# Kernel optimization log

Hardware: AMD Instinct MI355X
Metric: run time of the kernel (lower is better)

The kernel has to match this reference:

```python
import jax, jax.numpy as jnp
import numpy as np

N, S1, S2, H, D = 2, 4096, 4096, 8, 64

def setup_inputs() -> dict:
    key = jax.random.key(0)
    kq, kk, kv = jax.random.split(key, 3)
    queries = jax.random.normal(kq, (N, S1, H, D), dtype=jnp.float32)
    keys = jax.random.normal(kk, (N, S2, H, D), dtype=jnp.float32)
    values = jax.random.normal(kv, (N, S2, H, D), dtype=jnp.float32)
    q_mask = jnp.ones((N, S1), dtype=bool)
    kv_mask = jnp.ones((N, S2), dtype=bool)
    return {"queries": queries, "keys": keys, "values": values,
            "q_mask": q_mask, "kv_mask": kv_mask}

def reference(queries, keys, values, q_mask, kv_mask):
    # queries: [N,L,H,D], keys/values: [N,S,H,D], masks: [N,L]/[N,S]
    scale = 1.0 / jnp.sqrt(jnp.asarray(queries.shape[3], queries.dtype))
    q = queries * scale
    qk = jnp.einsum('nlhd,nshd->nlsh', q, keys)  # [N,L,S,H]
    valid = q_mask[:, :, None, None] & kv_mask[:, None, :, None]  # [N,L,S,1]
    qk = jnp.where(valid, qk, -jnp.inf)
    attn = jax.nn.softmax(qk, axis=2)  # softmax over S
    out = jnp.einsum('nlsh,nshd->nlhd', attn, values)  # [N,L,H,D]
    return out
```

## Files before the change

### kernel.cpp

```cpp
#include <hip/hip_runtime.h>
#include <hip/hip_bf16.h>
#include <stdint.h>

#define NB 2
#define S1d 4096
#define S2d 4096
#define NH 8
#define DH 64

typedef float f32x4 __attribute__((ext_vector_type(4)));
typedef float f32x16 __attribute__((ext_vector_type(16)));
typedef __bf16 bf16x8 __attribute__((ext_vector_type(8)));
typedef __bf16 bf16x2 __attribute__((ext_vector_type(2)));
typedef unsigned short u16x8 __attribute__((ext_vector_type(8)));

__device__ __forceinline__ unsigned short f2bf(float f) {
    union { float f; uint32_t u; } v; v.f = f;
    uint32_t u = v.u;
    return (unsigned short)((u + 0x7fffu + ((u >> 16) & 1u)) >> 16);
}

__device__ __forceinline__ __bf16 to_bf(float x) { return (__bf16)x; }

__device__ __forceinline__ float E2(float x) {
#if __has_builtin(__builtin_amdgcn_exp2f)
    return __builtin_amdgcn_exp2f(x);
#else
    return __expf(x * 0.69314718055994531f);
#endif
}

#define GLDS(gp, lp) __builtin_amdgcn_global_load_lds( \
    (const __attribute__((address_space(1))) uint32_t*)(gp), \
    (__attribute__((address_space(3))) uint32_t*)(lp), 16, 0, 0)

#define SWAP32(a, b) asm volatile("v_permlane32_swap_b32 %0, %1" : "+v"(a), "+v"(b))

__global__ void prep_kv(const float* __restrict__ k, const float* __restrict__ v,
                        unsigned short* __restrict__ kfb, unsigned short* __restrict__ vfb) {
    __shared__ unsigned short T[64][72];
    int mode = blockIdx.x >> 10;
    int bid  = blockIdx.x & 1023;
    int tile = bid & 63;
    int h    = (bid >> 6) & 7;
    int n    = bid >> 9;
    int t    = threadIdx.x;

    if (mode == 0) {
        int frag = t >> 5, l = t & 31;
        int st = frag >> 2, kt = frag & 3;
        int srow = tile * 64 + st * 32 + l;
        const float* src = k + (((size_t)n * S2d + srow) * NH + h) * DH + kt * 16;
        float4 x0 = *reinterpret_cast<const float4*>(src + 0);
        float4 x1 = *reinterpret_cast<const float4*>(src + 4);
        float4 x2 = *reinterpret_cast<const float4*>(src + 8);
        float4 x3 = *reinterpret_cast<const float4*>(src + 12);
        u16x8 lo, hi;
        lo[0] = f2bf(x0.x); lo[1] = f2bf(x0.y); lo[2] = f2bf(x0.z); lo[3] = f2bf(x0.w);
        lo[4] = f2bf(x1.x); lo[5] = f2bf(x1.y); lo[6] = f2bf(x1.z); lo[7] = f2bf(x1.w);
        hi[0] = f2bf(x2.x); hi[1] = f2bf(x2.y); hi[2] = f2bf(x2.z); hi[3] = f2bf(x2.w);
        hi[4] = f2bf(x3.x); hi[5] = f2bf(x3.y); hi[6] = f2bf(x3.z); hi[7] = f2bf(x3.w);
        size_t base = (((size_t)(n * NH + h) * 64 + tile) * 8 + frag) * 512;
        *reinterpret_cast<u16x8*>(kfb + base + l * 8)        = lo;
        *reinterpret_cast<u16x8*>(kfb + base + (l + 32) * 8) = hi;
    } else {
        {
            int r = t >> 2, dg = t & 3;
            const float* src = v + ((((size_t)n * S2d + tile * 64 + r) * NH + h) * DH) + dg * 16;
#pragma unroll
            for (int i = 0; i < 4; i++) {
                float4 x = *reinterpret_cast<const float4*>(src + i * 4);
                int d = dg * 16 + i * 4;
                T[d + 0][r] = f2bf(x.x);
                T[d + 1][r] = f2bf(x.y);
                T[d + 2][r] = f2bf(x.z);
                T[d + 3][r] = f2bf(x.w);
            }
        }
        __syncthreads();
        {
            int dh = t >> 7, kt = (t >> 5) & 3, l = t & 31;
            const u16x8* rp = reinterpret_cast<const u16x8*>(&T[dh * 32 + l][kt * 16]);
            u16x8 lo = rp[0], hi = rp[1];
            size_t base = (((size_t)(n * NH + h) * 64 + tile) * 8 + dh * 4 + kt) * 512;
            *reinterpret_cast<u16x8*>(vfb + base + l * 8)        = lo;
            *reinterpret_cast<u16x8*>(vfb + base + (l + 32) * 8) = hi;
        }
    }
}

#define QSCALE 0.1803368801111204f

union WU { uint32_t u; bf16x2 v; };
union FR { uint32_t u[4]; bf16x8 v; };

#define PACKPAIR(SS, B, OUT) do {                                        \
    WU a_, b_, c_, d_;                                                   \
    a_.v[0] = to_bf(SS[B+0]); a_.v[1] = to_bf(SS[B+1]);                  \
    c_.v[0] = to_bf(SS[B+4]); c_.v[1] = to_bf(SS[B+5]);                  \
    SWAP32(a_.u, c_.u);                                                  \
    b_.v[0] = to_bf(SS[B+2]); b_.v[1] = to_bf(SS[B+3]);                  \
    d_.v[0] = to_bf(SS[B+6]); d_.v[1] = to_bf(SS[B+7]);                  \
    SWAP32(b_.u, d_.u);                                                  \
    OUT.u[0] = a_.u; OUT.u[1] = b_.u; OUT.u[2] = c_.u; OUT.u[3] = d_.u;  \
  } while (0)

__global__ __launch_bounds__(256, 4) void flash(
    const float* __restrict__ q, const unsigned short* __restrict__ kfb,
    const unsigned short* __restrict__ vfb, float* __restrict__ out,
    float* __restrict__ pO1, float* __restrict__ sums) {

    __shared__ __align__(16) unsigned char smem[32768];

    int bid = blockIdx.x;
    int nh = (bid & 7) * 2 + ((bid >> 3) & 1);
    int qt = (bid >> 4) & 31;
    int kvhalf = bid >> 9;
    int n = nh >> 3, h = nh & 7;

    int tid = threadIdx.x;
    int lane = tid & 63, wid = tid >> 6;
    int l31 = lane & 31, h2 = lane >> 5;

    const unsigned short* kf = kfb + ((size_t)nh * 64 + kvhalf * 32) * 4096;
    const unsigned short* vf = vfb + ((size_t)nh * 64 + kvhalf * 32) * 4096;

    int g0 = wid * 128 + lane;
    int g1 = g0 + 64;
    const unsigned short* kg0 = kf + g0 * 8;
    const unsigned short* kg1 = kf + g1 * 8;
    const unsigned short* vg0 = vf + g0 * 8;
    const unsigned short* vg1 = vf + g1 * 8;

    {
        unsigned short* kl = (unsigned short*)smem;
        unsigned short* vl = (unsigned short*)(smem + 8192);
        GLDS(kg0, kl + g0 * 8);
        GLDS(kg1, kl + g1 * 8);
        GLDS(vg0, vl + g0 * 8);
        GLDS(vg1, vl + g1 * 8);
        kg0 += 4096; kg1 += 4096; vg0 += 4096; vg1 += 4096;
    }

    bf16x8 qf[4];
    {
        int qrow = qt * 128 + wid * 32 + l31;
        const float* qp = q + (((size_t)n * S1d + qrow) * NH + h) * DH;
#pragma unroll
        for (int kt = 0; kt < 4; kt++) {
            f32x4 x0 = *(const f32x4*)(qp + kt * 16 + h2 * 8);
            f32x4 x1 = *(const f32x4*)(qp + kt * 16 + h2 * 8 + 4);
            bf16x8 f;
#pragma unroll
            for (int j = 0; j < 4; j++) f[j] = to_bf(x0[j] * QSCALE);
#pragma unroll
            for (int j = 0; j < 4; j++) f[4 + j] = to_bf(x1[j] * QSCALE);
            qf[kt] = f;
        }
    }

    f32x16 o0, o1;
#pragma unroll
    for (int i = 0; i < 16; i++) { o0[i] = 0.f; o1[i] = 0.f; }
    float lsum = 0.f;

    __syncthreads();

    int lb = lane * 8;
    int cur = 0;
    for (int t = 0; t < 32; ++t) {
        if (t < 31) {
            unsigned short* kl = (unsigned short*)(smem + (cur ^ 1) * 16384);
            unsigned short* vl = (unsigned short*)(smem + (cur ^ 1) * 16384 + 8192);
            GLDS(kg0, kl + g0 * 8);
            GLDS(kg1, kl + g1 * 8);
            GLDS(vg0, vl + g0 * 8);
            GLDS(vg1, vl + g1 * 8);
            kg0 += 4096; kg1 += 4096; vg0 += 4096; vg1 += 4096;
        }

        const unsigned short* Kl = (const unsigned short*)(smem + cur * 16384);
        const unsigned short* Vl = (const unsigned short*)(smem + cur * 16384 + 8192);

        f32x16 s0, s1;
        __builtin_amdgcn_s_setprio(1);
        {
            bf16x8 k0 = *(const bf16x8*)&Kl[lb];
            bf16x8 k1 = *(const bf16x8*)&Kl[4 * 512 + lb];
            f32x16 z;
#pragma unroll
            for (int i = 0; i < 16; i++) z[i] = 0.f;
            s0 = __builtin_amdgcn_mfma_f32_32x32x16_bf16(k0, qf[0], z, 0, 0, 0);
            s1 = __builtin_amdgcn_mfma_f32_32x32x16_bf16(k1, qf[0], z, 0, 0, 0);
        }
#pragma unroll
        for (int kt = 1; kt < 4; kt++) {
            bf16x8 k0 = *(const bf16x8*)&Kl[kt * 512 + lb];
            bf16x8 k1 = *(const bf16x8*)&Kl[(4 + kt) * 512 + lb];
            s0 = __builtin_amdgcn_mfma_f32_32x32x16_bf16(k0, qf[kt], s0, 0, 0, 0);
            s1 = __builtin_amdgcn_mfma_f32_32x32x16_bf16(k1, qf[kt], s1, 0, 0, 0);
        }
        __builtin_amdgcn_s_setprio(0);

#pragma unroll
        for (int i = 0; i < 16; i++) { s0[i] = E2(s0[i]); s1[i] = E2(s1[i]); }

        {
            float ta[16];
#pragma unroll
            for (int i = 0; i < 16; i++) ta[i] = s0[i] + s1[i];
#pragma unroll
            for (int st = 8; st > 0; st >>= 1)
#pragma unroll
                for (int i = 0; i < 8; i++) if (i < st) ta[i] += ta[i + st];
            lsum += ta[0];
        }

        FR pf0, pf1, pf2, pf3;
        PACKPAIR(s0, 0, pf0);
        PACKPAIR(s0, 8, pf1);
        PACKPAIR(s1, 0, pf2);
        PACKPAIR(s1, 8, pf3);

        __builtin_amdgcn_s_setprio(1);
#pragma unroll
        for (int kt = 0; kt < 4; kt++) {
            bf16x8 v0 = *(const bf16x8*)&Vl[kt * 512 + lb];
            bf16x8 v1 = *(const bf16x8*)&Vl[(4 + kt) * 512 + lb];
            bf16x8 pw = (kt == 0) ? pf0.v : (kt == 1) ? pf1.v : (kt == 2) ? pf2.v : pf3.v;
            o0 = __builtin_amdgcn_mfma_f32_32x32x16_bf16(v0, pw, o0, 0, 0, 0);
            o1 = __builtin_amdgcn_mfma_f32_32x32x16_bf16(v1, pw, o1, 0, 0, 0);
        }
        __builtin_amdgcn_s_setprio(0);

        __syncthreads();
        cur ^= 1;
    }

    float tot = lsum + __shfl_xor(lsum, 32);
    int qrow = qt * 128 + wid * 32 + l31;
    if (h2 == 0)
        sums[(size_t)kvhalf * (NB * NH * S1d) + (size_t)nh * S1d + qrow] = tot;

    float* pO = kvhalf ? pO1 : out;
    float* rowp = pO + (((size_t)n * S1d + qrow) * NH + h) * DH;
#pragma unroll
    for (int r = 0; r < 16; r++) {
        int d0 = (r & 3) + 8 * (r >> 2) + 4 * h2;
        rowp[d0]      = o0[r];
        rowp[d0 + 32] = o1[r];
    }
}

__global__ void combine(float* __restrict__ out, const float* __restrict__ pO1,
                        const float* __restrict__ sums) {
    int bid = blockIdx.x;
    int nh = (bid & 7) * 2 + ((bid >> 3) & 1);
    int qc = bid >> 4;
    int n = nh >> 3, h = nh & 7;
    int t = threadIdx.x;
    int row = qc * 16 + (t >> 4), dg = t & 15;

    size_t off = ((((size_t)n * S1d + row) * NH + h) * DH) + dg * 4;
    f32x4 a = *(const f32x4*)(out + off);
    f32x4 b = *(const f32x4*)(pO1 + off);
    size_t si = (size_t)nh * S1d + row;
    float s = sums[si] + sums[(size_t)(NB * NH * S1d) + si];
    float inv = 1.0f / s;
    f32x4 r;
    r[0] = (a[0] + b[0]) * inv;
    r[1] = (a[1] + b[1]) * inv;
    r[2] = (a[2] + b[2]) * inv;
    r[3] = (a[3] + b[3]) * inv;
    *(f32x4*)(out + off) = r;
}

extern "C" void kernel_launch(void* const* d_in, const int* in_sizes, int n_in,
                              void* d_out, int out_size, void* d_ws, size_t ws_size,
                              hipStream_t stream) {
    const float* q = (const float*)d_in[0];
    const float* k = (const float*)d_in[1];
    const float* v = (const float*)d_in[2];
    float* out = (float*)d_out;

    unsigned short* kfb = (unsigned short*)d_ws;
    unsigned short* vfb = kfb + (size_t)NB * NH * S2d * DH;
    float* pO1  = (float*)(vfb + (size_t)NB * NH * S2d * DH);
    float* sums = pO1 + (size_t)NB * S1d * NH * DH;

    prep_kv<<<2048, 256, 0, stream>>>(k, v, kfb, vfb);
    flash<<<1024, 256, 0, stream>>>(q, kfb, vfb, out, pO1, sums);
    combine<<<4096, 256, 0, stream>>>(out, pO1, sums);
}
```

Before: 98.22 us.

## Fuse split-KV combine into flash kernel via in-block LDS reduction

Each block now runs 8 waves, and the two groups of 4 waves each process one half of the KV sequence for the same 128 query rows, with separate LDS double buffers. At the end, the second half writes its partial O and row sums to LDS, and the first half adds them, normalizes and writes the final output. This removes the separate combine kernel, the global partial-output and sums buffers, and their extra memory round trip. The risks are the larger 64KB LDS footprint per block and the changed launch bounds, which may tighten the register budget.

```diff
diff --git a/kernel.cpp b/kernel.cpp
--- a/kernel.cpp
+++ b/kernel.cpp
@@ -105,27 +105,28 @@
     OUT.u[0] = a_.u; OUT.u[1] = b_.u; OUT.u[2] = c_.u; OUT.u[3] = d_.u;  \
   } while (0)
 
-__global__ __launch_bounds__(256, 4) void flash(
+__global__ __launch_bounds__(512, 4) void flash(
     const float* __restrict__ q, const unsigned short* __restrict__ kfb,
-    const unsigned short* __restrict__ vfb, float* __restrict__ out,
-    float* __restrict__ pO1, float* __restrict__ sums) {
-
-    __shared__ __align__(16) unsigned char smem[32768];
+    const unsigned short* __restrict__ vfb, float* __restrict__ out) {
+
+    __shared__ __align__(16) unsigned char smem[65536];
 
     int bid = blockIdx.x;
     int nh = (bid & 7) * 2 + ((bid >> 3) & 1);
-    int qt = (bid >> 4) & 31;
-    int kvhalf = bid >> 9;
+    int qt = bid >> 4;
     int n = nh >> 3, h = nh & 7;
 
     int tid = threadIdx.x;
     int lane = tid & 63, wid = tid >> 6;
+    int w4 = wid & 3, kvhalf = wid >> 2;
     int l31 = lane & 31, h2 = lane >> 5;
 
     const unsigned short* kf = kfb + ((size_t)nh * 64 + kvhalf * 32) * 4096;
     const unsigned short* vf = vfb + ((size_t)nh * 64 + kvhalf * 32) * 4096;
 
-    int g0 = wid * 128 + lane;
+    unsigned char* pbase = smem + kvhalf * 32768;
+
+    int g0 = w4 * 128 + lane;
     int g1 = g0 + 64;
     const unsigned short* kg0 = kf + g0 * 8;
     const unsigned short* kg1 = kf + g1 * 8;
@@ -133,8 +134,8 @@
     const unsigned short* vg1 = vf + g1 * 8;
 
     {
-        unsigned short* kl = (unsigned short*)smem;
-        unsigned short* vl = (unsigned short*)(smem + 8192);
+        unsigned short* kl = (unsigned short*)pbase;
+        unsigned short* vl = (unsigned short*)(pbase + 8192);
         GLDS(kg0, kl + g0 * 8);
         GLDS(kg1, kl + g1 * 8);
         GLDS(vg0, vl + g0 * 8);
@@ -144,7 +145,7 @@
 
     bf16x8 qf[4];
     {
-        int qrow = qt * 128 + wid * 32 + l31;
+        int qrow = qt * 128 + w4 * 32 + l31;
         const float* qp = q + (((size_t)n * S1d + qrow) * NH + h) * DH;
 #pragma unroll
         for (int kt = 0; kt < 4; kt++) {
@@ -170,8 +171,8 @@
     int cur = 0;
     for (int t = 0; t < 32; ++t) {
         if (t < 31) {
-            unsigned short* kl = (unsigned short*)(smem + (cur ^ 1) * 16384);
-            unsigned short* vl = (unsigned short*)(smem + (cur ^ 1) * 16384 + 8192);
+            unsigned short* kl = (unsigned short*)(pbase + (cur ^ 1) * 16384);
+            unsigned short* vl = (unsigned short*)(pbase + (cur ^ 1) * 16384 + 8192);
             GLDS(kg0, kl + g0 * 8);
             GLDS(kg1, kl + g1 * 8);
             GLDS(vg0, vl + g0 * 8);
@@ -179,8 +180,8 @@
             kg0 += 4096; kg1 += 4096; vg0 += 4096; vg1 += 4096;
         }
 
-        const unsigned short* Kl = (const unsigned short*)(smem + cur * 16384);
-        const unsigned short* Vl = (const unsigned short*)(smem + cur * 16384 + 8192);
+        const unsigned short* Kl = (const unsigned short*)(pbase + cur * 16384);
+        const unsigned short* Vl = (const unsigned short*)(pbase + cur * 16384 + 8192);
 
         f32x16 s0, s1;
         __builtin_amdgcn_s_setprio(1);
@@ -238,41 +239,30 @@
     }
 
     float tot = lsum + __shfl_xor(lsum, 32);
-    int qrow = qt * 128 + wid * 32 + l31;
-    if (h2 == 0)
-        sums[(size_t)kvhalf * (NB * NH * S1d) + (size_t)nh * S1d + qrow] = tot;
-
-    float* pO = kvhalf ? pO1 : out;
-    float* rowp = pO + (((size_t)n * S1d + qrow) * NH + h) * DH;
-#pragma unroll
-    for (int r = 0; r < 16; r++) {
-        int d0 = (r & 3) + 8 * (r >> 2) + 4 * h2;
-        rowp[d0]      = o0[r];
-        rowp[d0 + 32] = o1[r];
-    }
-}
-
-__global__ void combine(float* __restrict__ out, const float* __restrict__ pO1,
-                        const float* __restrict__ sums) {
-    int bid = blockIdx.x;
-    int nh = (bid & 7) * 2 + ((bid >> 3) & 1);
-    int qc = bid >> 4;
-    int n = nh >> 3, h = nh & 7;
-    int t = threadIdx.x;
-    int row = qc * 16 + (t >> 4), dg = t & 15;
-
-    size_t off = ((((size_t)n * S1d + row) * NH + h) * DH) + dg * 4;
-    f32x4 a = *(const f32x4*)(out + off);
-    f32x4 b = *(const f32x4*)(pO1 + off);
-    size_t si = (size_t)nh * S1d + row;
-    float s = sums[si] + sums[(size_t)(NB * NH * S1d) + si];
-    float inv = 1.0f / s;
-    f32x4 r;
-    r[0] = (a[0] + b[0]) * inv;
-    r[1] = (a[1] + b[1]) * inv;
-    r[2] = (a[2] + b[2]) * inv;
-    r[3] = (a[3] + b[3]) * inv;
-    *(f32x4*)(out + off) = r;
+
+    float* sh = (float*)smem;
+    int sidx = (w4 * 64 + lane) * 34;
+    if (kvhalf == 1) {
+#pragma unroll
+        for (int r = 0; r < 16; r++) {
+            sh[sidx + r]      = o0[r];
+            sh[sidx + 16 + r] = o1[r];
+        }
+        sh[sidx + 32] = tot;
+    }
+    __syncthreads();
+
+    if (kvhalf == 0) {
+        float inv = 1.0f / (tot + sh[sidx + 32]);
+        int qrow = qt * 128 + w4 * 32 + l31;
+        float* rowp = out + (((size_t)n * S1d + qrow) * NH + h) * DH;
+#pragma unroll
+        for (int r = 0; r < 16; r++) {
+            int d0 = (r & 3) + 8 * (r >> 2) + 4 * h2;
+            rowp[d0]      = (o0[r] + sh[sidx + r])      * inv;
+            rowp[d0 + 32] = (o1[r] + sh[sidx + 16 + r]) * inv;
+        }
+    }
 }
 
 extern "C" void kernel_launch(void* const* d_in, const int* in_sizes, int n_in,
@@ -285,10 +275,7 @@
 
     unsigned short* kfb = (unsigned short*)d_ws;
     unsigned short* vfb = kfb + (size_t)NB * NH * S2d * DH;
-    float* pO1  = (float*)(vfb + (size_t)NB * NH * S2d * DH);
-    float* sums = pO1 + (size_t)NB * S1d * NH * DH;
 
     prep_kv<<<2048, 256, 0, stream>>>(k, v, kfb, vfb);
-    flash<<<1024, 256, 0, stream>>>(q, kfb, vfb, out, pO1, sums);
-    combine<<<4096, 256, 0, stream>>>(out, pO1, sums);
-}
+    flash<<<512, 512, 0, stream>>>(q, kfb, vfb, out);
+}
```

Result: faster. 89.30 us, median of 2 (-9.1%).
